# Kernel tuning notes

Hardware: AMD Instinct MI355X
Metric: run time of the kernel (lower is better)

The kernel has to match this reference:

```python
import jax, jax.numpy as jnp
import numpy as np

B = 131072
HID = 512
TEMB = 32
N_STEPS = 10


def time_embedding(t):
    # t: (B,) -> (B, TEMB) sinusoidal embedding
    half = TEMB // 2
    freqs = jnp.exp(-jnp.log(10000.0) * jnp.arange(half, dtype=jnp.float32) / half)
    args = t[:, None] * freqs[None, :]
    return jnp.concatenate([jnp.sin(args), jnp.cos(args)], axis=-1)


def setup_inputs() -> dict:
    key = jax.random.key(0)
    ks = jax.random.split(key, 9)
    def lin(k, fan_out, fan_in):
        s = 1.0 / np.sqrt(fan_in)
        kw, kb = jax.random.split(k)
        W = jax.random.uniform(kw, (fan_out, fan_in), jnp.float32, -s, s)
        b = jax.random.uniform(kb, (fan_out,), jnp.float32, -s, s)
        return W, b
    x = jax.random.normal(ks[0], (B, 2), jnp.float32)
    W0, b0 = lin(ks[1], HID, 2 + TEMB)
    W1, b1 = lin(ks[2], HID, HID)
    W2, b2 = lin(ks[3], HID, HID)
    # NOTE: original zero-inits last layer (trivial flow); use small random
    # weights so the Jacobian/log-det math is exercised non-trivially.
    W3 = 0.1 * jax.random.normal(ks[4], (2, HID), jnp.float32) / np.sqrt(HID)
    b3 = jnp.zeros((2,), jnp.float32)
    return {"x": x, "W0": W0, "b0": b0, "W1": W1, "b1": b1,
            "W2": W2, "b2": b2, "W3": W3, "b3": b3}


def reference(x, W0, b0, W1, b1, W2, b2, W3, b3):
    h_step = 1.0 / N_STEPS
    nb = x.shape[0]

    def vel(z, t):
        # z: (B,2), t: (B,) -> v: (B,2)
        h = jnp.concatenate([z, time_embedding(t)], axis=-1)
        h = jax.nn.silu(h @ W0.T + b0)
        h = jax.nn.silu(h @ W1.T + b1)
        h = jax.nn.silu(h @ W2.T + b2)
        return h @ W3.T + b3

    e0 = jnp.broadcast_to(jnp.array([1.0, 0.0], jnp.float32), (nb, 2))
    e1 = jnp.broadcast_to(jnp.array([0.0, 1.0], jnp.float32), (nb, 2))

    def step(carry, k):
        z, log_det = carry
        t = jnp.full((nb,), k * h_step, jnp.float32)
        f = lambda zz: vel(zz, t)
        # Batched JVPs give Jacobian columns: col0 = dv/dz0, col1 = dv/dz1
        v, col0 = jax.jvp(f, (z,), (e0,))
        _, col1 = jax.jvp(f, (z,), (e1,))
        det = (1.0 + h_step * col0[:, 0]) * (1.0 + h_step * col1[:, 1]) \
              - (h_step ** 2) * col1[:, 0] * col0[:, 1]
        log_det = log_det + jnp.log(jnp.clip(jnp.abs(det), 1e-8))
        z = z + h_step * v
        return (z, log_det), None

    ks = jnp.arange(N_STEPS, dtype=jnp.float32)
    (z, log_det), _ = jax.lax.scan(step, (x, jnp.zeros((nb,), jnp.float32)), ks)
    log_pz = -0.5 * jnp.sum(z ** 2 + jnp.log(2.0 * jnp.pi), axis=-1)
    return log_pz + log_det
```

## Files before the change

kernel.cpp:

```cpp
#include <hip/hip_runtime.h>
#include <hip/hip_bf16.h>
#include <math.h>


typedef float  f32x4  __attribute__((ext_vector_type(4)));
typedef float  f32x16 __attribute__((ext_vector_type(16)));
typedef __bf16 bf16x8 __attribute__((ext_vector_type(8)));

static __device__ __forceinline__ unsigned pkbf2(float a, float b) {
    unsigned short lo = __builtin_bit_cast(unsigned short, __float2bfloat16(a));
    unsigned short hi = __builtin_bit_cast(unsigned short, __float2bfloat16(b));
    return (unsigned)lo | ((unsigned)hi << 16);
}

__global__ void pack_w_kernel(const float* __restrict__ W,
                              __hip_bfloat16* __restrict__ out) {
    int i  = blockIdx.x * 512 + threadIdx.x;
    int c  = i >> 13;
    int nb = (i >> 9) & 15;
    int l  = (i >> 3) & 63;
    int j  = i & 7;
    int n  = nb * 32 + (l & 31);
    int k  = c * 16 + ((l >> 5) << 3) + j;
    out[i] = __float2bfloat16(W[n * 512 + k]);
}

__global__ void pack_w0_kernel(const float* __restrict__ W0,
                               float* __restrict__ w01) {
    int o = threadIdx.x;
    w01[o * 2 + 0] = W0[o * 34 + 0];
    w01[o * 2 + 1] = W0[o * 34 + 1];
}

__global__ void cstep_kernel(const float* __restrict__ W0,
                             const float* __restrict__ b0,
                             float* __restrict__ cst) {
    int k = blockIdx.x;
    int o = threadIdx.x;
    float t = (float)k * 0.1f;
    float acc = b0[o];
    #pragma unroll
    for (int j = 0; j < 16; ++j) {
        float f   = expf(-9.210340371976184f * (float)j / 16.0f);
        float arg = t * f;
        acc += W0[o * 34 + 2 + j]  * sinf(arg);
        acc += W0[o * 34 + 18 + j] * cosf(arg);
    }
    cst[k * 512 + o] = acc;
}

__global__ __launch_bounds__(1024)
void flow_kernel(const float* __restrict__ x,
                 const float* __restrict__ w01,
                 const float* __restrict__ cst,
                 const __hip_bfloat16* __restrict__ Wpk1,
                 const __hip_bfloat16* __restrict__ Wpk2,
                 const float* __restrict__ b1,
                 const float* __restrict__ b2,
                 const float* __restrict__ W3,
                 const float* __restrict__ b3v,
                 float* __restrict__ out)
{
    __shared__ __align__(16) __hip_bfloat16 Xbuf[96 * 512];
    __shared__ float zbuf[32][2];
    __shared__ float ldbuf[32];

    const int tid  = threadIdx.x;
    const int lane = tid & 63;
    const int wid  = tid >> 6;
    const int l31  = lane & 31;
    const int hi   = lane >> 5;
    const int n0w  = wid << 5;
    const int wgs  = blockIdx.x << 5;

    if (tid < 32) {
        zbuf[tid][0] = x[(wgs + tid) * 2 + 0];
        zbuf[tid][1] = x[(wgs + tid) * 2 + 1];
        ldbuf[tid]   = 0.0f;
    }

    const int rowb0 = l31 << 10;
    const int rowb1 = (32 + l31) << 10;
    const int rowb2 = (64 + l31) << 10;
    const int swzB  = (l31 & 7) << 4;
    const int hi16  = hi << 4;
    const int abase = (wid << 6) + lane;
    const uint4* Wp1 = (const uint4*)Wpk1;
    const uint4* Wp2 = (const uint4*)Wpk2;

    const int s0   = tid >> 5;
    const int t32  = tid & 31;
    const int swz0 = (s0 & 7) << 4;

    const char* xb = (const char*)Xbuf;

    __syncthreads();

    #pragma unroll 1
    for (int step = 0; step < 10; ++step) {
        {
            const float z0 = zbuf[s0][0];
            const float z1 = zbuf[s0][1];
            const float* cs = cst + (step << 9);
            char* base0 = (char*)Xbuf + (s0 << 10);
            #pragma unroll 1
            for (int m = 0; m < 2; ++m) {
                int ob = (t32 << 4) + (m << 3);
                const float4* wv4 = (const float4*)(w01 + (ob << 1));
                const float4* cv4 = (const float4*)(cs + ob);
                unsigned ph[4], p0[4], p1[4];
                #pragma unroll
                for (int jj = 0; jj < 4; ++jj) {
                    float4 wv = wv4[jj];
                    float4 cv = cv4[jj >> 1];
                    float c0 = (jj & 1) ? cv.z : cv.x;
                    float c1 = (jj & 1) ? cv.w : cv.y;
                    float a0  = fmaf(z0, wv.x, fmaf(z1, wv.y, c0));
                    float sg0 = 1.0f / (1.0f + __expf(-a0));
                    float h0  = a0 * sg0;
                    float sp0 = fmaf(h0, 1.0f - sg0, sg0);
                    float a1  = fmaf(z0, wv.z, fmaf(z1, wv.w, c1));
                    float sg1 = 1.0f / (1.0f + __expf(-a1));
                    float h1  = a1 * sg1;
                    float sp1 = fmaf(h1, 1.0f - sg1, sg1);
                    ph[jj] = pkbf2(h0, h1);
                    p0[jj] = pkbf2(sp0 * wv.x, sp1 * wv.z);
                    p1[jj] = pkbf2(sp0 * wv.y, sp1 * wv.w);
                }
                int off = (ob << 1) ^ swz0;
                uint4 vph = {ph[0], ph[1], ph[2], ph[3]};
                uint4 vp0 = {p0[0], p0[1], p0[2], p0[3]};
                uint4 vp1 = {p1[0], p1[1], p1[2], p1[3]};
                *(uint4*)(base0 + off)              = vph;
                *(uint4*)(base0 + (32 << 10) + off) = vp0;
                *(uint4*)(base0 + (64 << 10) + off) = vp1;
            }
        }
        __syncthreads();

        #pragma unroll 1
        for (int layer = 0; layer < 2; ++layer) {
            const uint4* __restrict__ Wp   = layer ? Wp2 : Wp1;
            const float* __restrict__ bias = layer ? b2  : b1;

            f32x16 acc0 = (f32x16)(0.0f);
            f32x16 acc1 = (f32x16)(0.0f);
            f32x16 acc2 = (f32x16)(0.0f);

            uint4 aCur = Wp[abase];
            #pragma unroll 2
            for (int c = 0; c < 32; ++c) {
                uint4 aNxt = Wp[abase + (((c + 1) & 31) << 10)];
                int kx = ((c << 5) | hi16) ^ swzB;
                bf16x8 bf0 = __builtin_bit_cast(bf16x8, *(const uint4*)(xb + rowb0 + kx));
                bf16x8 bf1 = __builtin_bit_cast(bf16x8, *(const uint4*)(xb + rowb1 + kx));
                bf16x8 bf2 = __builtin_bit_cast(bf16x8, *(const uint4*)(xb + rowb2 + kx));
                bf16x8 av  = __builtin_bit_cast(bf16x8, aCur);
                __builtin_amdgcn_s_setprio(1);
                acc0 = __builtin_amdgcn_mfma_f32_32x32x16_bf16(av, bf0, acc0, 0, 0, 0);
                acc1 = __builtin_amdgcn_mfma_f32_32x32x16_bf16(av, bf1, acc1, 0, 0, 0);
                acc2 = __builtin_amdgcn_mfma_f32_32x32x16_bf16(av, bf2, acc2, 0, 0, 0);
                __builtin_amdgcn_s_setprio(0);
                aCur = aNxt;
            }

            __syncthreads();

            {
                char* pb = (char*)Xbuf + (l31 << 10);
                #pragma unroll
                for (int q = 0; q < 4; ++q) {
                    int nq = n0w + 8 * q + 4 * hi;
                    f32x4 bq = *(const f32x4*)(bias + nq);
                    float hv[4], u0v[4], u1v[4];
                    #pragma unroll
                    for (int k = 0; k < 4; ++k) {
                        int reg = 4 * q + k;
                        float aa  = acc0[reg] + bq[k];
                        float sig = 1.0f / (1.0f + __expf(-aa));
                        float h   = aa * sig;
                        float sp  = fmaf(h, 1.0f - sig, sig);
                        hv[k]  = h;
                        u0v[k] = sp * acc1[reg];
                        u1v[k] = sp * acc2[reg];
                    }
                    int off = (nq << 1) ^ swzB;
                    uint2 vh = {pkbf2(hv[0],  hv[1]),  pkbf2(hv[2],  hv[3])};
                    uint2 v0 = {pkbf2(u0v[0], u0v[1]), pkbf2(u0v[2], u0v[3])};
                    uint2 v1 = {pkbf2(u1v[0], u1v[1]), pkbf2(u1v[2], u1v[3])};
                    *(uint2*)(pb + off)              = vh;
                    *(uint2*)(pb + (32 << 10) + off) = v0;
                    *(uint2*)(pb + (64 << 10) + off) = v1;
                }
            }
            __syncthreads();
        }

        {
            float d0 = 0.f, d1 = 0.f, d2 = 0.f, d3 = 0.f, d4 = 0.f, d5 = 0.f;
            #pragma unroll 1
            for (int p = 0; p < 2; ++p) {
                int eb = (t32 << 4) + (p << 3);
                const float4* wr0 = (const float4*)(W3 + eb);
                const float4* wr1 = (const float4*)(W3 + 512 + eb);
                float4 wa0 = wr0[0], wa1 = wr0[1];
                float4 wb0 = wr1[0], wb1 = wr1[1];
                #pragma unroll
                for (int st = 0; st < 3; ++st) {
                    int row = s0 + st * 32;
                    int off = (row << 10) + ((((t32 << 5) + (p << 4))) ^ swz0);
                    uint4 v = *(const uint4*)((const char*)Xbuf + off);
                    float e0 = __uint_as_float(v.x << 16);
                    float e1 = __uint_as_float(v.x & 0xffff0000u);
                    float e2 = __uint_as_float(v.y << 16);
                    float e3 = __uint_as_float(v.y & 0xffff0000u);
                    float e4 = __uint_as_float(v.z << 16);
                    float e5 = __uint_as_float(v.z & 0xffff0000u);
                    float e6 = __uint_as_float(v.w << 16);
                    float e7 = __uint_as_float(v.w & 0xffff0000u);
                    float sa = wa0.x * e0;
                    sa = fmaf(wa0.y, e1, sa); sa = fmaf(wa0.z, e2, sa);
                    sa = fmaf(wa0.w, e3, sa); sa = fmaf(wa1.x, e4, sa);
                    sa = fmaf(wa1.y, e5, sa); sa = fmaf(wa1.z, e6, sa);
                    sa = fmaf(wa1.w, e7, sa);
                    float sb = wb0.x * e0;
                    sb = fmaf(wb0.y, e1, sb); sb = fmaf(wb0.z, e2, sb);
                    sb = fmaf(wb0.w, e3, sb); sb = fmaf(wb1.x, e4, sb);
                    sb = fmaf(wb1.y, e5, sb); sb = fmaf(wb1.z, e6, sb);
                    sb = fmaf(wb1.w, e7, sb);
                    if      (st == 0) { d0 += sa; d1 += sb; }
                    else if (st == 1) { d2 += sa; d3 += sb; }
                    else              { d4 += sa; d5 += sb; }
                }
            }
            #pragma unroll
            for (int m = 1; m < 32; m <<= 1) {
                d0 += __shfl_xor(d0, m);
                d1 += __shfl_xor(d1, m);
                d2 += __shfl_xor(d2, m);
                d3 += __shfl_xor(d3, m);
                d4 += __shfl_xor(d4, m);
                d5 += __shfl_xor(d5, m);
            }
            if (t32 == 0) {
                float v0 = d0 + b3v[0];
                float v1 = d1 + b3v[1];
                float det = (1.0f + 0.1f * d2) * (1.0f + 0.1f * d5)
                          - 0.01f * d4 * d3;
                ldbuf[s0] += logf(fmaxf(fabsf(det), 1e-8f));
                zbuf[s0][0] += 0.1f * v0;
                zbuf[s0][1] += 0.1f * v1;
            }
        }
        __syncthreads();
    }

    if (tid < 32) {
        float z0 = zbuf[tid][0], z1 = zbuf[tid][1];
        out[wgs + tid] = -0.5f * (z0 * z0 + z1 * z1) - 1.8378770664093453f + ldbuf[tid];
    }
}

extern "C" void kernel_launch(void* const* d_in, const int* in_sizes, int n_in,
                              void* d_out, int out_size, void* d_ws, size_t ws_size,
                              hipStream_t stream) {
    const float* x  = (const float*)d_in[0];
    const float* W0 = (const float*)d_in[1];
    const float* b0 = (const float*)d_in[2];
    const float* W1 = (const float*)d_in[3];
    const float* b1 = (const float*)d_in[4];
    const float* W2 = (const float*)d_in[5];
    const float* b2 = (const float*)d_in[6];
    const float* W3 = (const float*)d_in[7];
    const float* b3 = (const float*)d_in[8];
    float* out = (float*)d_out;

    char* ws = (char*)d_ws;
    __hip_bfloat16* wpk1 = (__hip_bfloat16*)ws;
    __hip_bfloat16* wpk2 = (__hip_bfloat16*)(ws + (512u << 10));
    float*          cstp = (float*)(ws + (1024u << 10));
    float*          w01p = (float*)(ws + (1044u << 10));

    pack_w_kernel<<<512, 512, 0, stream>>>(W1, wpk1);
    pack_w_kernel<<<512, 512, 0, stream>>>(W2, wpk2);
    cstep_kernel<<<10, 512, 0, stream>>>(W0, b0, cstp);
    pack_w0_kernel<<<1, 512, 0, stream>>>(W0, w01p);
    flow_kernel<<<131072 / 32, 1024, 0, stream>>>(x, w01p, cstp, wpk1, wpk2,
                                                  b1, b2, W3, b3, out);
}
```

Baseline: 5.707 ms.

## Fuse final W3 projection into last hidden layer epilogue via per-wave partials

For the last hidden layer, the SiLU/JVP epilogue now multiplies directly by W3 in registers and reduces across lanes, writing per-wave partial sums into a small shared array. This replaces writing the bf16 activations to LDS, syncing, and re-reading them for a separate W3 dot-product pass. It removes one barrier and the LDS round trip, and the W3 dot products now use fp32 values instead of bf16-rounded ones. In exchange there is a serial 16-way partial reduction done by 32 threads.

```diff
diff --git a/kernel.cpp b/kernel.cpp
--- a/kernel.cpp
+++ b/kernel.cpp
@@ -64,6 +64,7 @@
     __shared__ __align__(16) __hip_bfloat16 Xbuf[96 * 512];
     __shared__ float zbuf[32][2];
     __shared__ float ldbuf[32];
+    __shared__ __align__(16) float part[16][32][8];
 
     const int tid  = threadIdx.x;
     const int lane = tid & 63;
@@ -164,9 +165,8 @@
                 aCur = aNxt;
             }
 
-            __syncthreads();
-
-            {
+            if (layer == 0) {
+                __syncthreads();
                 char* pb = (char*)Xbuf + (l31 << 10);
                 #pragma unroll
                 for (int q = 0; q < 4; ++q) {
@@ -184,7 +184,7 @@
                         u0v[k] = sp * acc1[reg];
                         u1v[k] = sp * acc2[reg];
                     }
-                    int off = (nq << 1) ^ swzB;
+                    int off = ((nq << 1) ^ swzB);
                     uint2 vh = {pkbf2(hv[0],  hv[1]),  pkbf2(hv[2],  hv[3])};
                     uint2 v0 = {pkbf2(u0v[0], u0v[1]), pkbf2(u0v[2], u0v[3])};
                     uint2 v1 = {pkbf2(u1v[0], u1v[1]), pkbf2(u1v[2], u1v[3])};
@@ -192,65 +192,64 @@
                     *(uint2*)(pb + (32 << 10) + off) = v0;
                     *(uint2*)(pb + (64 << 10) + off) = v1;
                 }
-            }
-            __syncthreads();
+                __syncthreads();
+            } else {
+                float q0 = 0.f, q1 = 0.f, q2 = 0.f, q3 = 0.f, q4 = 0.f, q5 = 0.f;
+                #pragma unroll
+                for (int q = 0; q < 4; ++q) {
+                    int nq = n0w + 8 * q + 4 * hi;
+                    f32x4 bq = *(const f32x4*)(bias + nq);
+                    f32x4 w0 = *(const f32x4*)(W3 + nq);
+                    f32x4 w1 = *(const f32x4*)(W3 + 512 + nq);
+                    #pragma unroll
+                    for (int k = 0; k < 4; ++k) {
+                        int reg = 4 * q + k;
+                        float aa  = acc0[reg] + bq[k];
+                        float sig = 1.0f / (1.0f + __expf(-aa));
+                        float h   = aa * sig;
+                        float sp  = fmaf(h, 1.0f - sig, sig);
+                        float u0  = sp * acc1[reg];
+                        float u1  = sp * acc2[reg];
+                        q0 = fmaf(w0[k], h,  q0);
+                        q1 = fmaf(w1[k], h,  q1);
+                        q2 = fmaf(w0[k], u0, q2);
+                        q3 = fmaf(w1[k], u0, q3);
+                        q4 = fmaf(w0[k], u1, q4);
+                        q5 = fmaf(w1[k], u1, q5);
+                    }
+                }
+                q0 += __shfl_xor(q0, 32);
+                q1 += __shfl_xor(q1, 32);
+                q2 += __shfl_xor(q2, 32);
+                q3 += __shfl_xor(q3, 32);
+                q4 += __shfl_xor(q4, 32);
+                q5 += __shfl_xor(q5, 32);
+                if (hi == 0) {
+                    float* pp = &part[wid][l31][0];
+                    pp[0] = q0; pp[1] = q1; pp[2] = q2;
+                    pp[3] = q3; pp[4] = q4; pp[5] = q5;
+                }
+                __syncthreads();
+            }
         }
 
-        {
-            float d0 = 0.f, d1 = 0.f, d2 = 0.f, d3 = 0.f, d4 = 0.f, d5 = 0.f;
-            #pragma unroll 1
-            for (int p = 0; p < 2; ++p) {
-                int eb = (t32 << 4) + (p << 3);
-                const float4* wr0 = (const float4*)(W3 + eb);
-                const float4* wr1 = (const float4*)(W3 + 512 + eb);
-                float4 wa0 = wr0[0], wa1 = wr0[1];
-                float4 wb0 = wr1[0], wb1 = wr1[1];
-                #pragma unroll
-                for (int st = 0; st < 3; ++st) {
-                    int row = s0 + st * 32;
-                    int off = (row << 10) + ((((t32 << 5) + (p << 4))) ^ swz0);
-                    uint4 v = *(const uint4*)((const char*)Xbuf + off);
-                    float e0 = __uint_as_float(v.x << 16);
-                    float e1 = __uint_as_float(v.x & 0xffff0000u);
-                    float e2 = __uint_as_float(v.y << 16);
-                    float e3 = __uint_as_float(v.y & 0xffff0000u);
-                    float e4 = __uint_as_float(v.z << 16);
-                    float e5 = __uint_as_float(v.z & 0xffff0000u);
-                    float e6 = __uint_as_float(v.w << 16);
-                    float e7 = __uint_as_float(v.w & 0xffff0000u);
-                    float sa = wa0.x * e0;
-                    sa = fmaf(wa0.y, e1, sa); sa = fmaf(wa0.z, e2, sa);
-                    sa = fmaf(wa0.w, e3, sa); sa = fmaf(wa1.x, e4, sa);
-                    sa = fmaf(wa1.y, e5, sa); sa = fmaf(wa1.z, e6, sa);
-                    sa = fmaf(wa1.w, e7, sa);
-                    float sb = wb0.x * e0;
-                    sb = fmaf(wb0.y, e1, sb); sb = fmaf(wb0.z, e2, sb);
-                    sb = fmaf(wb0.w, e3, sb); sb = fmaf(wb1.x, e4, sb);
-                    sb = fmaf(wb1.y, e5, sb); sb = fmaf(wb1.z, e6, sb);
-                    sb = fmaf(wb1.w, e7, sb);
-                    if      (st == 0) { d0 += sa; d1 += sb; }
-                    else if (st == 1) { d2 += sa; d3 += sb; }
-                    else              { d4 += sa; d5 += sb; }
-                }
-            }
+        if (tid < 32) {
+            float s0v = 0.f, s1v = 0.f, s2v = 0.f, s3v = 0.f, s4v = 0.f, s5v = 0.f;
             #pragma unroll
-            for (int m = 1; m < 32; m <<= 1) {
-                d0 += __shfl_xor(d0, m);
-                d1 += __shfl_xor(d1, m);
-                d2 += __shfl_xor(d2, m);
-                d3 += __shfl_xor(d3, m);
-                d4 += __shfl_xor(d4, m);
-                d5 += __shfl_xor(d5, m);
-            }
-            if (t32 == 0) {
-                float v0 = d0 + b3v[0];
-                float v1 = d1 + b3v[1];
-                float det = (1.0f + 0.1f * d2) * (1.0f + 0.1f * d5)
-                          - 0.01f * d4 * d3;
-                ldbuf[s0] += logf(fmaxf(fabsf(det), 1e-8f));
-                zbuf[s0][0] += 0.1f * v0;
-                zbuf[s0][1] += 0.1f * v1;
-            }
+            for (int w = 0; w < 16; ++w) {
+                const float* pp = &part[w][tid][0];
+                f32x4 a = *(const f32x4*)(pp);
+                f32x4 b = *(const f32x4*)(pp + 4);
+                s0v += a[0]; s1v += a[1]; s2v += a[2];
+                s3v += a[3]; s4v += b[0]; s5v += b[1];
+            }
+            float v0 = s0v + b3v[0];
+            float v1 = s1v + b3v[1];
+            float det = (1.0f + 0.1f * s2v) * (1.0f + 0.1f * s5v)
+                      - 0.01f * s4v * s3v;
+            ldbuf[tid] += logf(fmaxf(fabsf(det), 1e-8f));
+            zbuf[tid][0] += 0.1f * v0;
+            zbuf[tid][1] += 0.1f * v1;
         }
         __syncthreads();
     }
```

Measured after the change: 5.324 ms. -6.7%, faster.
